# Optimization experiments

Hardware: AMD Instinct MI355X
Metric: run time of the kernel (lower is better)

## Reference

```python
import jax, jax.numpy as jnp
import numpy as np

N = 100000
NEG_SLOPE = 0.2
EPS = 1e-16


def _gat_layer(x, W, a_src, a_dst, b, src, dst, heads, dim, concat):
    # Linear projection -> [N, H, D]
    h = (x @ W).reshape(x.shape[0], heads, dim)
    # Per-node attention logits [N, H]
    al_src = jnp.sum(h * a_src[None], axis=-1)
    al_dst = jnp.sum(h * a_dst[None], axis=-1)
    # Per-edge logits, leaky relu (negative_slope=0.2)
    e = al_src[src] + al_dst[dst]                      # [E, H]
    e = jnp.where(e >= 0, e, NEG_SLOPE * e)
    # Scatter softmax over destination neighborhoods
    emax = jax.ops.segment_max(e, dst, num_segments=N)  # [N, H]
    ee = jnp.exp(e - emax[dst])
    denom = jax.ops.segment_sum(ee, dst, num_segments=N)
    alpha = ee / (denom[dst] + EPS)                    # [E, H]
    # Weighted scatter-add aggregation
    msg = h[src] * alpha[:, :, None]                   # [E, H, D]
    out = jax.ops.segment_sum(msg, dst, num_segments=N)  # [N, H, D]
    if concat:
        out = out.reshape(N, heads * dim)
    else:
        out = out.mean(axis=1)
    return out + b


def setup_inputs() -> dict:
    key = jax.random.key(0)
    ks = jax.random.split(key, 10)
    F_in, hid, H, C = 500, 8, 8, 3
    E = 3200000
    x = jax.random.normal(ks[0], (N, F_in), dtype=jnp.float32)
    edge_index = jax.random.randint(ks[1], (2, E), 0, N, dtype=jnp.int64)
    s1 = (1.0 / np.sqrt(F_in)).astype(np.float32)
    s2 = (1.0 / np.sqrt(hid * H)).astype(np.float32)
    return {
        "x": x,
        "edge_index": edge_index,
        "W1": jax.random.normal(ks[2], (F_in, H * hid), dtype=jnp.float32) * s1,
        "att_src1": jax.random.normal(ks[3], (H, hid), dtype=jnp.float32),
        "att_dst1": jax.random.normal(ks[4], (H, hid), dtype=jnp.float32),
        "b1": jnp.zeros((H * hid,), dtype=jnp.float32),
        "W2": jax.random.normal(ks[5], (H * hid, C), dtype=jnp.float32) * s2,
        "att_src2": jax.random.normal(ks[6], (1, C), dtype=jnp.float32),
        "att_dst2": jax.random.normal(ks[7], (1, C), dtype=jnp.float32),
        "b2": jnp.zeros((C,), dtype=jnp.float32),
    }


def reference(x, edge_index, W1, att_src1, att_dst1, b1, W2, att_src2, att_dst2, b2):
    # Add self-loops (PyG GATConv default)
    loop = jnp.arange(N, dtype=edge_index.dtype)
    src = jnp.concatenate([edge_index[0], loop])
    dst = jnp.concatenate([edge_index[1], loop])
    # Layer 1: 8 heads, concat -> [N, 64], ELU
    h = _gat_layer(x, W1, att_src1, att_dst1, b1, src, dst, heads=8, dim=8, concat=True)
    h = jax.nn.elu(h)
    # Layer 2: 1 head, no concat -> [N, 3]
    out = _gat_layer(h, W2, att_src2, att_dst2, b2, src, dst, heads=1, dim=3, concat=False)
    return out, jax.nn.log_softmax(out, axis=1)
```

## Files before the change

kernel.cpp:

```cpp
#include <hip/hip_runtime.h>
#include <hip/hip_bf16.h>


#define F_IN 500
#define HEADS 8
#define HID 8
#define HD 64
#define CLS 3
#define NEG 0.2f
#define EPSV 1e-16f
#define LOG2E 1.44269504088896340736f

#define NBLK_H 256
#define NBKT_MAX 3136

typedef __attribute__((ext_vector_type(8))) short short8v;
typedef __attribute__((ext_vector_type(4))) float f32x4;

__device__ inline short bfs(float v) {
    __hip_bfloat16 b = __float2bfloat16(v);
    return *(short*)&b;
}

__device__ inline int ld_edge(const void* ei, long idx, int is64) {
    return is64 ? (int)((const long long*)ei)[idx] : ((const int*)ei)[idx];
}

__global__ void k_prepW(const float* __restrict__ W1, ushort* __restrict__ W1b2,
                        const int* __restrict__ ei, int* __restrict__ flag) {
    if (blockIdx.x == 0 && threadIdx.x == 0) {
        int z = 0;
        for (int i = 1; i < 16; i += 2) z += (ei[i] == 0) ? 1 : 0;
        *flag = (z == 8) ? 1 : 0;
    }
    int i = blockIdx.x * 256 + threadIdx.x;
    if (i >= 16 * 64 * 32) return;
    int ks = i >> 11;
    int c = (i >> 5) & 63;
    int st = i & 31;
    int q = (st >> 3) ^ ((c >> 1) & 3);
    int k = ks * 32 + q * 8 + (st & 7);
    float v = (k < F_IN) ? W1[k * HD + c] : 0.f;
    __hip_bfloat16 b = __float2bfloat16(v);
    W1b2[i] = *(ushort*)&b;
}

__device__ __forceinline__ void g1_stage(const float* __restrict__ x,
        const ushort* __restrict__ W1b2, char* smem, int buf, int ks,
        int rowb, int N, int lane, int w) {
    const int k0 = ks * 32;
    {
        const ushort* srcB = W1b2 + ks * 2048 + (w * 64 + lane) * 8;
        char* dstB = smem + 16384 + buf * 4096 + w * 1024;
        __builtin_amdgcn_global_load_lds(
            (const __attribute__((address_space(1))) void*)srcB,
            (__attribute__((address_space(3))) void*)dstB, 16, 0, 0);
    }
#pragma unroll
    for (int i = 0; i < 2; ++i) {
        int vt = i * 256 + w * 64 + lane;
        int row = vt >> 3;
        int c = (vt & 7) ^ (row & 7);
        int ke = k0 + c * 4; if (ke > 496) ke = 496;
        int rowg = rowb + row; if (rowg >= N) rowg = N - 1;
        const float* srcA = x + (long)rowg * F_IN + ke;
        char* dstA = smem + buf * 8192 + i * 4096 + w * 1024;
        __builtin_amdgcn_global_load_lds(
            (const __attribute__((address_space(1))) void*)srcA,
            (__attribute__((address_space(3))) void*)dstA, 16, 0, 0);
    }
}

__global__ __launch_bounds__(256) void k_fatA(const float* __restrict__ x,
        const ushort* __restrict__ W1b2,
        const float* __restrict__ asrc, const float* __restrict__ adst,
        float* __restrict__ als, float* __restrict__ ald,
        ushort* __restrict__ h1b, int N,
        const void* ei, int E, int nbkt, int* __restrict__ ghist,
        const int* __restrict__ flag) {
    __shared__ char smem[24576];
    int gB = (N + 63) >> 6;
    int t = threadIdx.x;

    if ((int)blockIdx.x >= gB) {
        int hb = blockIdx.x - gB;
        int* h = (int*)smem;
        int tot = E + N;
        int epb = (tot + NBLK_H - 1) / NBLK_H;
        int e0 = hb * epb, e1 = min(tot, e0 + epb);
        for (int i = t; i < nbkt; i += 256) h[i] = 0;
        __syncthreads();
        int is64 = *flag;
        for (int e = e0 + t; e < e1; e += 256) {
            int dst = (e < E) ? ld_edge(ei, (long)E + e, is64) : (e - E);
            atomicAdd(&h[dst >> 5], 1);
        }
        __syncthreads();
        for (int i = t; i < nbkt; i += 256)
            ghist[hb * nbkt + i] = h[i];
        return;
    }

    int lane = t & 63;
    int w = t >> 6;
    int l16 = lane & 15, oct = lane >> 4;
    int rowb = blockIdx.x * 64;

    f32x4 acc0 = {0.f, 0.f, 0.f, 0.f};
    f32x4 acc1 = {0.f, 0.f, 0.f, 0.f};
    f32x4 acc2 = {0.f, 0.f, 0.f, 0.f};
    f32x4 acc3 = {0.f, 0.f, 0.f, 0.f};

    g1_stage(x, W1b2, smem, 0, 0, rowb, N, lane, w);
    __syncthreads();

    int rl = w * 16 + l16;
    int asw = l16 & 7;
    int bsw = (l16 >> 1) & 3;

    for (int ks = 0; ks < 16; ++ks) {
        int cur = ks & 1;
        if (ks < 15)
            g1_stage(x, W1b2, smem, cur ^ 1, ks + 1, rowb, N, lane, w);
        const char* Ab = smem + cur * 8192;
        const char* Bb = smem + 16384 + cur * 4096;
        float4 x0 = *reinterpret_cast<const float4*>(
            Ab + rl * 128 + ((2 * oct + 0) ^ asw) * 16);
        float4 x1 = *reinterpret_cast<const float4*>(
            Ab + rl * 128 + ((2 * oct + 1) ^ asw) * 16);
        short8v a;
        a[0] = bfs(x0.x); a[1] = bfs(x0.y); a[2] = bfs(x0.z); a[3] = bfs(x0.w);
        a[4] = bfs(x1.x); a[5] = bfs(x1.y); a[6] = bfs(x1.z); a[7] = bfs(x1.w);
        short8v b0 = *reinterpret_cast<const short8v*>(
            Bb + (0 * 16 + l16) * 64 + (oct ^ bsw) * 16);
        short8v b1 = *reinterpret_cast<const short8v*>(
            Bb + (1 * 16 + l16) * 64 + (oct ^ bsw) * 16);
        short8v b2 = *reinterpret_cast<const short8v*>(
            Bb + (2 * 16 + l16) * 64 + (oct ^ bsw) * 16);
        short8v b3 = *reinterpret_cast<const short8v*>(
            Bb + (3 * 16 + l16) * 64 + (oct ^ bsw) * 16);
        acc0 = __builtin_amdgcn_mfma_f32_16x16x32_bf16(a, b0, acc0, 0, 0, 0);
        acc1 = __builtin_amdgcn_mfma_f32_16x16x32_bf16(a, b1, acc1, 0, 0, 0);
        acc2 = __builtin_amdgcn_mfma_f32_16x16x32_bf16(a, b2, acc2, 0, 0, 0);
        acc3 = __builtin_amdgcn_mfma_f32_16x16x32_bf16(a, b3, acc3, 0, 0, 0);
        __syncthreads();
    }

    float* fs = (float*)smem;
#pragma unroll
    for (int r = 0; r < 4; ++r) {
        int rl_ = w * 16 + oct * 4 + r;
        fs[rl_ * 64 + l16 +  0] = acc0[r];
        fs[rl_ * 64 + l16 + 16] = acc1[r];
        fs[rl_ * 64 + l16 + 32] = acc2[r];
        fs[rl_ * 64 + l16 + 48] = acc3[r];
    }
    __syncthreads();
#pragma unroll
    for (int j = t; j < 512; j += 256) {
        int row = j >> 3, h = j & 7;
        int gn = rowb + row;
        if (gn < N) {
            const float* hp = fs + row * 64 + h * 8;
            float4 v0 = *reinterpret_cast<const float4*>(hp);
            float4 v1 = *reinterpret_cast<const float4*>(hp + 4);
            const float* s = asrc + h * 8;
            const float* d = adst + h * 8;
            float s1 = v0.x * s[0] + v0.y * s[1] + v0.z * s[2] + v0.w * s[3]
                     + v1.x * s[4] + v1.y * s[5] + v1.z * s[6] + v1.w * s[7];
            float s2 = v0.x * d[0] + v0.y * d[1] + v0.z * d[2] + v0.w * d[3]
                     + v1.x * d[4] + v1.y * d[5] + v1.z * d[6] + v1.w * d[7];
            als[gn * 8 + h] = s1 * LOG2E;
            ald[gn * 8 + h] = s2 * LOG2E;
            ushort hb[8];
            hb[0] = (ushort)bfs(v0.x); hb[1] = (ushort)bfs(v0.y);
            hb[2] = (ushort)bfs(v0.z); hb[3] = (ushort)bfs(v0.w);
            hb[4] = (ushort)bfs(v1.x); hb[5] = (ushort)bfs(v1.y);
            hb[6] = (ushort)bfs(v1.z); hb[7] = (ushort)bfs(v1.w);
            *reinterpret_cast<uint4*>(h1b + (long)gn * HD + h * 8) =
                *reinterpret_cast<const uint4*>(hb);
        }
    }
}


__global__ void k_bsum(const int* __restrict__ ghist, int* __restrict__ colsum, int nbkt) {
    int b = blockIdx.x * 256 + threadIdx.x;
    if (b >= nbkt) return;
    int s = 0;
    for (int i = 0; i < NBLK_H; i++) s += ghist[i * nbkt + b];
    colsum[b] = s;
}

__global__ __launch_bounds__(256) void k_bscan2(const int* __restrict__ colsum,
        int* __restrict__ boff, int nbkt) {
    __shared__ int part[256];
    int per = (nbkt + 255) / 256;
    int t = threadIdx.x;
    int lo = t * per, hi = min(nbkt, lo + per);
    int s = 0;
    for (int i = lo; i < hi; i++) s += colsum[i];
    part[t] = s;
    __syncthreads();
    for (int off = 1; off < 256; off <<= 1) {
        int v = (t >= off) ? part[t - off] : 0;
        __syncthreads();
        part[t] += v;
        __syncthreads();
    }
    int run = (t > 0) ? part[t - 1] : 0;
    for (int i = lo; i < hi; i++) { boff[i] = run; run += colsum[i]; }
    if (t == 255) boff[nbkt] = part[255];
}

__global__ void k_bapply(int* __restrict__ ghist, const int* __restrict__ boff, int nbkt) {
    int b = blockIdx.x * 256 + threadIdx.x;
    if (b >= nbkt) return;
    int run = boff[b];
    for (int i = 0; i < NBLK_H; i++) {
        int v = ghist[i * nbkt + b];
        ghist[i * nbkt + b] = run;
        run += v;
    }
}

__global__ __launch_bounds__(256) void k_scatter(const void* ei, int E, int N, int nbkt,
        const int* __restrict__ ghist, uint* __restrict__ pairs, const int* flag) {
    __shared__ int cur[NBKT_MAX];
    int tot = E + N;
    int epb = (tot + NBLK_H - 1) / NBLK_H;
    int e0 = blockIdx.x * epb, e1 = min(tot, e0 + epb);
    for (int i = threadIdx.x; i < nbkt; i += 256) cur[i] = ghist[blockIdx.x * nbkt + i];
    __syncthreads();
    int is64 = *flag;
    for (int e = e0 + threadIdx.x; e < e1; e += 256) {
        int src, dst;
        if (e < E) { src = ld_edge(ei, e, is64); dst = ld_edge(ei, (long)E + e, is64); }
        else { src = dst = e - E; }
        int pos = atomicAdd(&cur[dst >> 5], 1);
        pairs[pos] = ((uint)src << 5) | (uint)(dst & 31);
    }
}

__global__ __launch_bounds__(256) void k_fill3(const uint* __restrict__ pairs,
        const int* __restrict__ boff, int* __restrict__ rowptr,
        int* __restrict__ csr, int N, int nbkt) {
    __shared__ int cnt[32];
    __shared__ int base[32];
    __shared__ int cur[32];
    int b = blockIdx.x;
    int t = threadIdx.x;
    if (t < 32) { cnt[t] = 0; cur[t] = 0; }
    __syncthreads();
    int p0 = boff[b], p1 = boff[b + 1];
    for (int p = p0 + t; p < p1; p += 256)
        atomicAdd(&cnt[pairs[p] & 31], 1);
    __syncthreads();
    if (t < 32) {
        int pre = 0;
#pragma unroll
        for (int i = 0; i < 32; i++) pre += (i < t) ? cnt[i] : 0;
        base[t] = p0 + pre;
        int n = b * 32 + t;
        if (n < N) rowptr[n] = base[t];
    }
    if (b == 0 && t == 0) rowptr[N] = boff[nbkt];
    __syncthreads();
    for (int p = p0 + t; p < p1; p += 256) {
        uint v = pairs[p];
        int lo = v & 31;
        int pos = base[lo] + atomicAdd(&cur[lo], 1);
        csr[pos] = (int)(v >> 5);
    }
}

__global__ __launch_bounds__(256) void k_agg1(const int* __restrict__ rowptr,
        const int* __restrict__ csr, const ushort* __restrict__ h1b,
        const float* __restrict__ als, const float* __restrict__ ald,
        const float* __restrict__ b1, const float* __restrict__ W2,
        const float* __restrict__ as2, const float* __restrict__ ad2,
        float* __restrict__ h2p, float* __restrict__ als2,
        float* __restrict__ ald2, int N) {
    int n = blockIdx.x * 4 + (threadIdx.x >> 6);
    if (n >= N) return;
    int lane = threadIdx.x & 63;
    int es = lane >> 3;
    int h = lane & 7;
    float aldh = ald[n * HEADS + h];
    int rs = rowptr[n], re = rowptr[n + 1];

    float acc[4][8];
    float den[4] = {0.f, 0.f, 0.f, 0.f};
#pragma unroll
    for (int q = 0; q < 4; ++q)
#pragma unroll
        for (int j = 0; j < 8; ++j) acc[q][j] = 0.f;

    int jb = rs;
    for (; jb + 32 <= re; jb += 32) {
        int s[4]; float e[4]; float p[4]; uint4 u[4];
#pragma unroll
        for (int q = 0; q < 4; ++q) s[q] = csr[jb + q * 8 + es];
#pragma unroll
        for (int q = 0; q < 4; ++q) {
            e[q] = als[s[q] * HEADS + h] + aldh;
            u[q] = *reinterpret_cast<const uint4*>(h1b + (long)s[q] * HD + h * 8);
        }
#pragma unroll
        for (int q = 0; q < 4; ++q) {
            e[q] = fmaxf(e[q], NEG * e[q]);
            p[q] = exp2f(e[q]);
        }
#pragma unroll
        for (int q = 0; q < 4; ++q) {
            acc[q][0] += p[q] * __uint_as_float(u[q].x << 16);
            acc[q][1] += p[q] * __uint_as_float(u[q].x & 0xffff0000u);
            acc[q][2] += p[q] * __uint_as_float(u[q].y << 16);
            acc[q][3] += p[q] * __uint_as_float(u[q].y & 0xffff0000u);
            acc[q][4] += p[q] * __uint_as_float(u[q].z << 16);
            acc[q][5] += p[q] * __uint_as_float(u[q].z & 0xffff0000u);
            acc[q][6] += p[q] * __uint_as_float(u[q].w << 16);
            acc[q][7] += p[q] * __uint_as_float(u[q].w & 0xffff0000u);
            den[q] += p[q];
        }
    }
    for (; jb + 16 <= re; jb += 16) {
        int s[2]; float e[2]; float p[2]; uint4 u[2];
#pragma unroll
        for (int q = 0; q < 2; ++q) s[q] = csr[jb + q * 8 + es];
#pragma unroll
        for (int q = 0; q < 2; ++q) {
            e[q] = als[s[q] * HEADS + h] + aldh;
            u[q] = *reinterpret_cast<const uint4*>(h1b + (long)s[q] * HD + h * 8);
        }
#pragma unroll
        for (int q = 0; q < 2; ++q) {
            e[q] = fmaxf(e[q], NEG * e[q]);
            p[q] = exp2f(e[q]);
        }
#pragma unroll
        for (int q = 0; q < 2; ++q) {
            acc[q][0] += p[q] * __uint_as_float(u[q].x << 16);
            acc[q][1] += p[q] * __uint_as_float(u[q].x & 0xffff0000u);
            acc[q][2] += p[q] * __uint_as_float(u[q].y << 16);
            acc[q][3] += p[q] * __uint_as_float(u[q].y & 0xffff0000u);
            acc[q][4] += p[q] * __uint_as_float(u[q].z << 16);
            acc[q][5] += p[q] * __uint_as_float(u[q].z & 0xffff0000u);
            acc[q][6] += p[q] * __uint_as_float(u[q].w << 16);
            acc[q][7] += p[q] * __uint_as_float(u[q].w & 0xffff0000u);
            den[q] += p[q];
        }
    }
    for (; jb < re; jb += 8) {
        int eidx = jb + es;
        bool valid = (eidx < re);
        int s = csr[valid ? eidx : rs];
        float e = als[s * HEADS + h] + aldh;
        e = fmaxf(e, NEG * e);
        float p = valid ? exp2f(e) : 0.f;
        uint4 u = *reinterpret_cast<const uint4*>(h1b + (long)s * HD + h * 8);
        acc[0][0] += p * __uint_as_float(u.x << 16);
        acc[0][1] += p * __uint_as_float(u.x & 0xffff0000u);
        acc[0][2] += p * __uint_as_float(u.y << 16);
        acc[0][3] += p * __uint_as_float(u.y & 0xffff0000u);
        acc[0][4] += p * __uint_as_float(u.z << 16);
        acc[0][5] += p * __uint_as_float(u.z & 0xffff0000u);
        acc[0][6] += p * __uint_as_float(u.w << 16);
        acc[0][7] += p * __uint_as_float(u.w & 0xffff0000u);
        den[0] += p;
    }
    float a0 = (acc[0][0] + acc[1][0]) + (acc[2][0] + acc[3][0]);
    float a1 = (acc[0][1] + acc[1][1]) + (acc[2][1] + acc[3][1]);
    float a2 = (acc[0][2] + acc[1][2]) + (acc[2][2] + acc[3][2]);
    float a3 = (acc[0][3] + acc[1][3]) + (acc[2][3] + acc[3][3]);
    float a4 = (acc[0][4] + acc[1][4]) + (acc[2][4] + acc[3][4]);
    float a5 = (acc[0][5] + acc[1][5]) + (acc[2][5] + acc[3][5]);
    float a6 = (acc[0][6] + acc[1][6]) + (acc[2][6] + acc[3][6]);
    float a7 = (acc[0][7] + acc[1][7]) + (acc[2][7] + acc[3][7]);
    float dn = (den[0] + den[1]) + (den[2] + den[3]);
#pragma unroll
    for (int off = 8; off < 64; off <<= 1) {
        dn += __shfl_xor(dn, off);
        a0 += __shfl_xor(a0, off); a1 += __shfl_xor(a1, off);
        a2 += __shfl_xor(a2, off); a3 += __shfl_xor(a3, off);
        a4 += __shfl_xor(a4, off); a5 += __shfl_xor(a5, off);
        a6 += __shfl_xor(a6, off); a7 += __shfl_xor(a7, off);
    }
    float sel = (es < 4)
        ? ((es < 2) ? ((es == 0) ? a0 : a1) : ((es == 2) ? a2 : a3))
        : ((es < 6) ? ((es == 4) ? a4 : a5) : ((es == 6) ? a6 : a7));
    int d = h * 8 + es;
    float o = sel / (dn + EPSV) + b1[d];
    o = (o > 0.f) ? o : __expf(o) - 1.f;
    float p0 = o * W2[d * CLS + 0];
    float p1 = o * W2[d * CLS + 1];
    float p2 = o * W2[d * CLS + 2];
#pragma unroll
    for (int off = 1; off < 64; off <<= 1) {
        p0 += __shfl_xor(p0, off);
        p1 += __shfl_xor(p1, off);
        p2 += __shfl_xor(p2, off);
    }
    if (lane == 0) {
        *reinterpret_cast<float4*>(h2p + (long)n * 4) = make_float4(p0, p1, p2, 0.f);
        als2[n] = (p0 * as2[0] + p1 * as2[1] + p2 * as2[2]) * LOG2E;
        ald2[n] = (p0 * ad2[0] + p1 * ad2[1] + p2 * ad2[2]) * LOG2E;
    }
}

__global__ __launch_bounds__(256) void k_agg2(const int* __restrict__ rowptr,
        const int* __restrict__ csr, const float* __restrict__ h2p,
        const float* __restrict__ als2v, const float* __restrict__ ald2v,
        const float* __restrict__ b2, float* __restrict__ out, int N) {
    int n = blockIdx.x * 8 + (threadIdx.x >> 5);
    if (n >= N) return;
    int lane = threadIdx.x & 31;
    float aldv = ald2v[n];
    int rs = rowptr[n], re = rowptr[n + 1];
    float sum = 0.f, a0 = 0.f, a1 = 0.f, a2 = 0.f;
    for (int j = rs + lane; j < re; j += 32) {
        int s = csr[j];
        float e = als2v[s] + aldv;
        e = fmaxf(e, NEG * e);
        float p = exp2f(e);
        float4 hv = *reinterpret_cast<const float4*>(h2p + (long)s * 4);
        sum += p;
        a0 += p * hv.x;
        a1 += p * hv.y;
        a2 += p * hv.z;
    }
#pragma unroll
    for (int off = 1; off < 32; off <<= 1) {
        sum += __shfl_xor(sum, off);
        a0 += __shfl_xor(a0, off);
        a1 += __shfl_xor(a1, off);
        a2 += __shfl_xor(a2, off);
    }
    if (lane == 0) {
        float d = sum + EPSV;
        float v0 = a0 / d + b2[0], v1 = a1 / d + b2[1], v2 = a2 / d + b2[2];
        float mx = fmaxf(v0, fmaxf(v1, v2));
        float se = __expf(v0 - mx) + __expf(v1 - mx) + __expf(v2 - mx);
        float ls = mx + __logf(se);
        out[n * CLS + 0] = v0; out[n * CLS + 1] = v1; out[n * CLS + 2] = v2;
        long o2 = (long)N * CLS;
        out[o2 + n * CLS + 0] = v0 - ls;
        out[o2 + n * CLS + 1] = v1 - ls;
        out[o2 + n * CLS + 2] = v2 - ls;
    }
}

extern "C" void kernel_launch(void* const* d_in, const int* in_sizes, int n_in,
                              void* d_out, int out_size, void* d_ws, size_t ws_size,
                              hipStream_t stream) {
    const float* x   = (const float*)d_in[0];
    const void*  ei  = d_in[1];
    const float* W1  = (const float*)d_in[2];
    const float* as1 = (const float*)d_in[3];
    const float* ad1 = (const float*)d_in[4];
    const float* b1  = (const float*)d_in[5];
    const float* W2  = (const float*)d_in[6];
    const float* as2 = (const float*)d_in[7];
    const float* ad2 = (const float*)d_in[8];
    const float* b2  = (const float*)d_in[9];
    int N = in_sizes[0] / F_IN;
    int E = in_sizes[1] / 2;
    int tot = E + N;
    int nbkt = (N + 31) >> 5;

    char* w = (char*)d_ws;
    auto alloc = [&](size_t bytes) -> char* {
        char* p = w; w += (bytes + 255) & ~size_t(255); return p;
    };
    ushort* h1b    = (ushort*)alloc((size_t)N * HD * 2);
    float*  als1   = (float*)alloc((size_t)N * HEADS * 4);
    float*  ald1   = (float*)alloc((size_t)N * HEADS * 4);
    int*    rowptr = (int*)alloc((size_t)(N + 1) * 4);
    int*    csr    = (int*)alloc((size_t)tot * 4);
    float*  h2p    = (float*)alloc((size_t)N * 4 * 4);
    float*  als2   = (float*)alloc((size_t)N * 4);
    float*  ald2   = (float*)alloc((size_t)N * 4);
    ushort* W1b2   = (ushort*)alloc((size_t)16 * 64 * 32 * 2);
    int*    flag   = (int*)alloc(256);
    uint*   pairs  = (uint*)alloc((size_t)tot * 4);
    int*    ghist  = (int*)alloc((size_t)NBLK_H * nbkt * 4);
    int*    colsum = (int*)alloc((size_t)nbkt * 4);
    int*    boff   = (int*)alloc((size_t)(nbkt + 1) * 4);

    int gB = (N + 63) / 64;
    k_prepW<<<(16 * 64 * 32 + 255) / 256, 256, 0, stream>>>(W1, W1b2, (const int*)ei, flag);
    k_fatA<<<gB + NBLK_H, 256, 0, stream>>>(x, W1b2, as1, ad1, als1, ald1, h1b, N,
                                            ei, E, nbkt, ghist, flag);
    k_bsum<<<(nbkt + 255) / 256, 256, 0, stream>>>(ghist, colsum, nbkt);
    k_bscan2<<<1, 256, 0, stream>>>(colsum, boff, nbkt);
    k_bapply<<<(nbkt + 255) / 256, 256, 0, stream>>>(ghist, boff, nbkt);
    k_scatter<<<NBLK_H, 256, 0, stream>>>(ei, E, N, nbkt, ghist, pairs, flag);
    k_fill3<<<nbkt, 256, 0, stream>>>(pairs, boff, rowptr, csr, N, nbkt);
    k_agg1<<<(N + 3) / 4, 256, 0, stream>>>(rowptr, csr, h1b, als1, ald1, b1,
                                            W2, as2, ad2, h2p, als2, ald2, N);
    k_agg2<<<(N + 7) / 8, 256, 0, stream>>>(rowptr, csr, h2p, als2, ald2, b2,
                                            (float*)d_out, N);
}
```

Before: 306.7 us.

## Recompute source attention logits from gathered bf16 features instead of gathering als

Layer 1 no longer precomputes and stores per-node source logits. The aggregation kernel instead recomputes them from the bf16 h1 vector it already gathers, as an 8-wide dot product with att_src. This removes one dependent random gather per edge and the als write/read traffic, at the cost of extra FMAs and slightly different numerics, since bf16 features now feed the logits. Layer 2 packs its source logit into the unused fourth slot of h2p, so one float4 gather serves both values. The 16-edge remainder loop is also dropped, so leftover edges now go through the 8-wide tail loop.

```diff
diff --git a/kernel.cpp b/kernel.cpp
--- a/kernel.cpp
+++ b/kernel.cpp
@@ -73,8 +73,8 @@
 
 __global__ __launch_bounds__(256) void k_fatA(const float* __restrict__ x,
         const ushort* __restrict__ W1b2,
-        const float* __restrict__ asrc, const float* __restrict__ adst,
-        float* __restrict__ als, float* __restrict__ ald,
+        const float* __restrict__ adst,
+        float* __restrict__ ald,
         ushort* __restrict__ h1b, int N,
         const void* ei, int E, int nbkt, int* __restrict__ ghist,
         const int* __restrict__ flag) {
@@ -164,13 +164,9 @@
             const float* hp = fs + row * 64 + h * 8;
             float4 v0 = *reinterpret_cast<const float4*>(hp);
             float4 v1 = *reinterpret_cast<const float4*>(hp + 4);
-            const float* s = asrc + h * 8;
             const float* d = adst + h * 8;
-            float s1 = v0.x * s[0] + v0.y * s[1] + v0.z * s[2] + v0.w * s[3]
-                     + v1.x * s[4] + v1.y * s[5] + v1.z * s[6] + v1.w * s[7];
             float s2 = v0.x * d[0] + v0.y * d[1] + v0.z * d[2] + v0.w * d[3]
                      + v1.x * d[4] + v1.y * d[5] + v1.z * d[6] + v1.w * d[7];
-            als[gn * 8 + h] = s1 * LOG2E;
             ald[gn * 8 + h] = s2 * LOG2E;
             ushort hb[8];
             hb[0] = (ushort)bfs(v0.x); hb[1] = (ushort)bfs(v0.y);
@@ -276,17 +272,19 @@
 
 __global__ __launch_bounds__(256) void k_agg1(const int* __restrict__ rowptr,
         const int* __restrict__ csr, const ushort* __restrict__ h1b,
-        const float* __restrict__ als, const float* __restrict__ ald,
+        const float* __restrict__ asrc, const float* __restrict__ ald,
         const float* __restrict__ b1, const float* __restrict__ W2,
         const float* __restrict__ as2, const float* __restrict__ ad2,
-        float* __restrict__ h2p, float* __restrict__ als2,
-        float* __restrict__ ald2, int N) {
+        float* __restrict__ h2p, float* __restrict__ ald2, int N) {
     int n = blockIdx.x * 4 + (threadIdx.x >> 6);
     if (n >= N) return;
     int lane = threadIdx.x & 63;
     int es = lane >> 3;
     int h = lane & 7;
     float aldh = ald[n * HEADS + h];
+    float asc[8];
+#pragma unroll
+    for (int j = 0; j < 8; ++j) asc[j] = asrc[h * 8 + j] * LOG2E;
     int rs = rowptr[n], re = rowptr[n + 1];
 
     float acc[4][8];
@@ -298,75 +296,56 @@
 
     int jb = rs;
     for (; jb + 32 <= re; jb += 32) {
-        int s[4]; float e[4]; float p[4]; uint4 u[4];
+        int s[4]; uint4 u[4];
 #pragma unroll
         for (int q = 0; q < 4; ++q) s[q] = csr[jb + q * 8 + es];
 #pragma unroll
+        for (int q = 0; q < 4; ++q)
+            u[q] = *reinterpret_cast<const uint4*>(h1b + (long)s[q] * HD + h * 8);
+#pragma unroll
         for (int q = 0; q < 4; ++q) {
-            e[q] = als[s[q] * HEADS + h] + aldh;
-            u[q] = *reinterpret_cast<const uint4*>(h1b + (long)s[q] * HD + h * 8);
-        }
-#pragma unroll
-        for (int q = 0; q < 4; ++q) {
-            e[q] = fmaxf(e[q], NEG * e[q]);
-            p[q] = exp2f(e[q]);
-        }
-#pragma unroll
-        for (int q = 0; q < 4; ++q) {
-            acc[q][0] += p[q] * __uint_as_float(u[q].x << 16);
-            acc[q][1] += p[q] * __uint_as_float(u[q].x & 0xffff0000u);
-            acc[q][2] += p[q] * __uint_as_float(u[q].y << 16);
-            acc[q][3] += p[q] * __uint_as_float(u[q].y & 0xffff0000u);
-            acc[q][4] += p[q] * __uint_as_float(u[q].z << 16);
-            acc[q][5] += p[q] * __uint_as_float(u[q].z & 0xffff0000u);
-            acc[q][6] += p[q] * __uint_as_float(u[q].w << 16);
-            acc[q][7] += p[q] * __uint_as_float(u[q].w & 0xffff0000u);
-            den[q] += p[q];
-        }
-    }
-    for (; jb + 16 <= re; jb += 16) {
-        int s[2]; float e[2]; float p[2]; uint4 u[2];
-#pragma unroll
-        for (int q = 0; q < 2; ++q) s[q] = csr[jb + q * 8 + es];
-#pragma unroll
-        for (int q = 0; q < 2; ++q) {
-            e[q] = als[s[q] * HEADS + h] + aldh;
-            u[q] = *reinterpret_cast<const uint4*>(h1b + (long)s[q] * HD + h * 8);
-        }
-#pragma unroll
-        for (int q = 0; q < 2; ++q) {
-            e[q] = fmaxf(e[q], NEG * e[q]);
-            p[q] = exp2f(e[q]);
-        }
-#pragma unroll
-        for (int q = 0; q < 2; ++q) {
-            acc[q][0] += p[q] * __uint_as_float(u[q].x << 16);
-            acc[q][1] += p[q] * __uint_as_float(u[q].x & 0xffff0000u);
-            acc[q][2] += p[q] * __uint_as_float(u[q].y << 16);
-            acc[q][3] += p[q] * __uint_as_float(u[q].y & 0xffff0000u);
-            acc[q][4] += p[q] * __uint_as_float(u[q].z << 16);
-            acc[q][5] += p[q] * __uint_as_float(u[q].z & 0xffff0000u);
-            acc[q][6] += p[q] * __uint_as_float(u[q].w << 16);
-            acc[q][7] += p[q] * __uint_as_float(u[q].w & 0xffff0000u);
-            den[q] += p[q];
+            float f0 = __uint_as_float(u[q].x << 16);
+            float f1 = __uint_as_float(u[q].x & 0xffff0000u);
+            float f2 = __uint_as_float(u[q].y << 16);
+            float f3 = __uint_as_float(u[q].y & 0xffff0000u);
+            float f4 = __uint_as_float(u[q].z << 16);
+            float f5 = __uint_as_float(u[q].z & 0xffff0000u);
+            float f6 = __uint_as_float(u[q].w << 16);
+            float f7 = __uint_as_float(u[q].w & 0xffff0000u);
+            float e = ((f0 * asc[0] + f1 * asc[1]) + (f2 * asc[2] + f3 * asc[3]))
+                    + ((f4 * asc[4] + f5 * asc[5]) + (f6 * asc[6] + f7 * asc[7]))
+                    + aldh;
+            e = fmaxf(e, NEG * e);
+            float p = exp2f(e);
+            acc[q][0] += p * f0; acc[q][1] += p * f1;
+            acc[q][2] += p * f2; acc[q][3] += p * f3;
+            acc[q][4] += p * f4; acc[q][5] += p * f5;
+            acc[q][6] += p * f6; acc[q][7] += p * f7;
+            den[q] += p;
         }
     }
     for (; jb < re; jb += 8) {
         int eidx = jb + es;
         bool valid = (eidx < re);
         int s = csr[valid ? eidx : rs];
-        float e = als[s * HEADS + h] + aldh;
+        uint4 u = *reinterpret_cast<const uint4*>(h1b + (long)s * HD + h * 8);
+        float f0 = __uint_as_float(u.x << 16);
+        float f1 = __uint_as_float(u.x & 0xffff0000u);
+        float f2 = __uint_as_float(u.y << 16);
+        float f3 = __uint_as_float(u.y & 0xffff0000u);
+        float f4 = __uint_as_float(u.z << 16);
+        float f5 = __uint_as_float(u.z & 0xffff0000u);
+        float f6 = __uint_as_float(u.w << 16);
+        float f7 = __uint_as_float(u.w & 0xffff0000u);
+        float e = ((f0 * asc[0] + f1 * asc[1]) + (f2 * asc[2] + f3 * asc[3]))
+                + ((f4 * asc[4] + f5 * asc[5]) + (f6 * asc[6] + f7 * asc[7]))
+                + aldh;
         e = fmaxf(e, NEG * e);
         float p = valid ? exp2f(e) : 0.f;
-        uint4 u = *reinterpret_cast<const uint4*>(h1b + (long)s * HD + h * 8);
-        acc[0][0] += p * __uint_as_float(u.x << 16);
-        acc[0][1] += p * __uint_as_float(u.x & 0xffff0000u);
-        acc[0][2] += p * __uint_as_float(u.y << 16);
-        acc[0][3] += p * __uint_as_float(u.y & 0xffff0000u);
-        acc[0][4] += p * __uint_as_float(u.z << 16);
-        acc[0][5] += p * __uint_as_float(u.z & 0xffff0000u);
-        acc[0][6] += p * __uint_as_float(u.w << 16);
-        acc[0][7] += p * __uint_as_float(u.w & 0xffff0000u);
+        acc[0][0] += p * f0; acc[0][1] += p * f1;
+        acc[0][2] += p * f2; acc[0][3] += p * f3;
+        acc[0][4] += p * f4; acc[0][5] += p * f5;
+        acc[0][6] += p * f6; acc[0][7] += p * f7;
         den[0] += p;
     }
     float a0 = (acc[0][0] + acc[1][0]) + (acc[2][0] + acc[3][0]);
@@ -402,15 +381,16 @@
         p2 += __shfl_xor(p2, off);
     }
     if (lane == 0) {
-        *reinterpret_cast<float4*>(h2p + (long)n * 4) = make_float4(p0, p1, p2, 0.f);
-        als2[n] = (p0 * as2[0] + p1 * as2[1] + p2 * as2[2]) * LOG2E;
+        float als2v = (p0 * as2[0] + p1 * as2[1] + p2 * as2[2]) * LOG2E;
+        *reinterpret_cast<float4*>(h2p + (long)n * 4) =
+            make_float4(p0, p1, p2, als2v);
         ald2[n] = (p0 * ad2[0] + p1 * ad2[1] + p2 * ad2[2]) * LOG2E;
     }
 }
 
 __global__ __launch_bounds__(256) void k_agg2(const int* __restrict__ rowptr,
         const int* __restrict__ csr, const float* __restrict__ h2p,
-        const float* __restrict__ als2v, const float* __restrict__ ald2v,
+        const float* __restrict__ ald2v,
         const float* __restrict__ b2, float* __restrict__ out, int N) {
     int n = blockIdx.x * 8 + (threadIdx.x >> 5);
     if (n >= N) return;
@@ -420,10 +400,10 @@
     float sum = 0.f, a0 = 0.f, a1 = 0.f, a2 = 0.f;
     for (int j = rs + lane; j < re; j += 32) {
         int s = csr[j];
-        float e = als2v[s] + aldv;
+        float4 hv = *reinterpret_cast<const float4*>(h2p + (long)s * 4);
+        float e = hv.w + aldv;
         e = fmaxf(e, NEG * e);
         float p = exp2f(e);
-        float4 hv = *reinterpret_cast<const float4*>(h2p + (long)s * 4);
         sum += p;
         a0 += p * hv.x;
         a1 += p * hv.y;
@@ -473,12 +453,10 @@
         char* p = w; w += (bytes + 255) & ~size_t(255); return p;
     };
     ushort* h1b    = (ushort*)alloc((size_t)N * HD * 2);
-    float*  als1   = (float*)alloc((size_t)N * HEADS * 4);
     float*  ald1   = (float*)alloc((size_t)N * HEADS * 4);
     int*    rowptr = (int*)alloc((size_t)(N + 1) * 4);
     int*    csr    = (int*)alloc((size_t)tot * 4);
     float*  h2p    = (float*)alloc((size_t)N * 4 * 4);
-    float*  als2   = (float*)alloc((size_t)N * 4);
     float*  ald2   = (float*)alloc((size_t)N * 4);
     ushort* W1b2   = (ushort*)alloc((size_t)16 * 64 * 32 * 2);
     int*    flag   = (int*)alloc(256);
@@ -489,15 +467,15 @@
 
     int gB = (N + 63) / 64;
     k_prepW<<<(16 * 64 * 32 + 255) / 256, 256, 0, stream>>>(W1, W1b2, (const int*)ei, flag);
-    k_fatA<<<gB + NBLK_H, 256, 0, stream>>>(x, W1b2, as1, ad1, als1, ald1, h1b, N,
+    k_fatA<<<gB + NBLK_H, 256, 0, stream>>>(x, W1b2, ad1, ald1, h1b, N,
                                             ei, E, nbkt, ghist, flag);
     k_bsum<<<(nbkt + 255) / 256, 256, 0, stream>>>(ghist, colsum, nbkt);
     k_bscan2<<<1, 256, 0, stream>>>(colsum, boff, nbkt);
     k_bapply<<<(nbkt + 255) / 256, 256, 0, stream>>>(ghist, boff, nbkt);
     k_scatter<<<NBLK_H, 256, 0, stream>>>(ei, E, N, nbkt, ghist, pairs, flag);
     k_fill3<<<nbkt, 256, 0, stream>>>(pairs, boff, rowptr, csr, N, nbkt);
-    k_agg1<<<(N + 3) / 4, 256, 0, stream>>>(rowptr, csr, h1b, als1, ald1, b1,
-                                            W2, as2, ad2, h2p, als2, ald2, N);
-    k_agg2<<<(N + 7) / 8, 256, 0, stream>>>(rowptr, csr, h2p, als2, ald2, b2,
+    k_agg1<<<(N + 3) / 4, 256, 0, stream>>>(rowptr, csr, h1b, as1, ald1, b1,
+                                            W2, as2, ad2, h2p, ald2, N);
+    k_agg2<<<(N + 7) / 8, 256, 0, stream>>>(rowptr, csr, h2p, ald2, b2,
                                             (float*)d_out, N);
 }
```

After: 314.5 us. 1.03x slower.

## Use half-wavefront per node in agg1 and pack als2 into h2p padding

Applied to the files above, without the earlier changes.

The layer-1 aggregation now assigns 32 lanes per destination node instead of 64, processing two nodes per wavefront with 4 edge slots per head. Average degree is about 32, so the old full-wave path mostly hit the remainder loops. The change also drops a shuffle stage and splits the final reduction across two feature columns per lane. The layer-2 source logit is stored in the unused fourth float of h2p, so agg2 gets it from the same float4 gather and one separate array and its random loads go away.

```diff
diff --git a/kernel.cpp b/kernel.cpp
--- a/kernel.cpp
+++ b/kernel.cpp
@@ -279,15 +279,17 @@
         const float* __restrict__ als, const float* __restrict__ ald,
         const float* __restrict__ b1, const float* __restrict__ W2,
         const float* __restrict__ as2, const float* __restrict__ ad2,
-        float* __restrict__ h2p, float* __restrict__ als2,
-        float* __restrict__ ald2, int N) {
-    int n = blockIdx.x * 4 + (threadIdx.x >> 6);
-    if (n >= N) return;
+        float* __restrict__ h2p, float* __restrict__ ald2, int N) {
     int lane = threadIdx.x & 63;
-    int es = lane >> 3;
+    int wid = threadIdx.x >> 6;
+    int half = lane >> 5;
+    int n = blockIdx.x * 8 + wid * 2 + half;
+    bool act = (n < N);
+    int nc = act ? n : (N - 1);
+    int es = (lane >> 3) & 3;
     int h = lane & 7;
-    float aldh = ald[n * HEADS + h];
-    int rs = rowptr[n], re = rowptr[n + 1];
+    float aldh = ald[nc * HEADS + h];
+    int rs = rowptr[nc], re = rowptr[nc + 1];
 
     float acc[4][8];
     float den[4] = {0.f, 0.f, 0.f, 0.f};
@@ -297,10 +299,10 @@
         for (int j = 0; j < 8; ++j) acc[q][j] = 0.f;
 
     int jb = rs;
-    for (; jb + 32 <= re; jb += 32) {
+    for (; jb + 16 <= re; jb += 16) {
         int s[4]; float e[4]; float p[4]; uint4 u[4];
 #pragma unroll
-        for (int q = 0; q < 4; ++q) s[q] = csr[jb + q * 8 + es];
+        for (int q = 0; q < 4; ++q) s[q] = csr[jb + q * 4 + es];
 #pragma unroll
         for (int q = 0; q < 4; ++q) {
             e[q] = als[s[q] * HEADS + h] + aldh;
@@ -324,34 +326,7 @@
             den[q] += p[q];
         }
     }
-    for (; jb + 16 <= re; jb += 16) {
-        int s[2]; float e[2]; float p[2]; uint4 u[2];
-#pragma unroll
-        for (int q = 0; q < 2; ++q) s[q] = csr[jb + q * 8 + es];
-#pragma unroll
-        for (int q = 0; q < 2; ++q) {
-            e[q] = als[s[q] * HEADS + h] + aldh;
-            u[q] = *reinterpret_cast<const uint4*>(h1b + (long)s[q] * HD + h * 8);
-        }
-#pragma unroll
-        for (int q = 0; q < 2; ++q) {
-            e[q] = fmaxf(e[q], NEG * e[q]);
-            p[q] = exp2f(e[q]);
-        }
-#pragma unroll
-        for (int q = 0; q < 2; ++q) {
-            acc[q][0] += p[q] * __uint_as_float(u[q].x << 16);
-            acc[q][1] += p[q] * __uint_as_float(u[q].x & 0xffff0000u);
-            acc[q][2] += p[q] * __uint_as_float(u[q].y << 16);
-            acc[q][3] += p[q] * __uint_as_float(u[q].y & 0xffff0000u);
-            acc[q][4] += p[q] * __uint_as_float(u[q].z << 16);
-            acc[q][5] += p[q] * __uint_as_float(u[q].z & 0xffff0000u);
-            acc[q][6] += p[q] * __uint_as_float(u[q].w << 16);
-            acc[q][7] += p[q] * __uint_as_float(u[q].w & 0xffff0000u);
-            den[q] += p[q];
-        }
-    }
-    for (; jb < re; jb += 8) {
+    for (; jb < re; jb += 4) {
         int eidx = jb + es;
         bool valid = (eidx < re);
         int s = csr[valid ? eidx : rs];
@@ -379,38 +354,41 @@
     float a7 = (acc[0][7] + acc[1][7]) + (acc[2][7] + acc[3][7]);
     float dn = (den[0] + den[1]) + (den[2] + den[3]);
 #pragma unroll
-    for (int off = 8; off < 64; off <<= 1) {
+    for (int off = 8; off <= 16; off <<= 1) {
         dn += __shfl_xor(dn, off);
         a0 += __shfl_xor(a0, off); a1 += __shfl_xor(a1, off);
         a2 += __shfl_xor(a2, off); a3 += __shfl_xor(a3, off);
         a4 += __shfl_xor(a4, off); a5 += __shfl_xor(a5, off);
         a6 += __shfl_xor(a6, off); a7 += __shfl_xor(a7, off);
     }
-    float sel = (es < 4)
-        ? ((es < 2) ? ((es == 0) ? a0 : a1) : ((es == 2) ? a2 : a3))
-        : ((es < 6) ? ((es == 4) ? a4 : a5) : ((es == 6) ? a6 : a7));
-    int d = h * 8 + es;
-    float o = sel / (dn + EPSV) + b1[d];
-    o = (o > 0.f) ? o : __expf(o) - 1.f;
-    float p0 = o * W2[d * CLS + 0];
-    float p1 = o * W2[d * CLS + 1];
-    float p2 = o * W2[d * CLS + 2];
-#pragma unroll
-    for (int off = 1; off < 64; off <<= 1) {
+    float sel_a = (es < 2) ? ((es == 0) ? a0 : a1) : ((es == 2) ? a2 : a3);
+    float sel_b = (es < 2) ? ((es == 0) ? a4 : a5) : ((es == 2) ? a6 : a7);
+    int da = h * 8 + es, db = da + 4;
+    float inv = 1.f / (dn + EPSV);
+    float oa = sel_a * inv + b1[da];
+    float ob = sel_b * inv + b1[db];
+    oa = (oa > 0.f) ? oa : __expf(oa) - 1.f;
+    ob = (ob > 0.f) ? ob : __expf(ob) - 1.f;
+    float p0 = oa * W2[da * CLS + 0] + ob * W2[db * CLS + 0];
+    float p1 = oa * W2[da * CLS + 1] + ob * W2[db * CLS + 1];
+    float p2 = oa * W2[da * CLS + 2] + ob * W2[db * CLS + 2];
+#pragma unroll
+    for (int off = 1; off <= 16; off <<= 1) {
         p0 += __shfl_xor(p0, off);
         p1 += __shfl_xor(p1, off);
         p2 += __shfl_xor(p2, off);
     }
-    if (lane == 0) {
-        *reinterpret_cast<float4*>(h2p + (long)n * 4) = make_float4(p0, p1, p2, 0.f);
-        als2[n] = (p0 * as2[0] + p1 * as2[1] + p2 * as2[2]) * LOG2E;
+    if ((lane & 31) == 0 && act) {
+        float als2v = (p0 * as2[0] + p1 * as2[1] + p2 * as2[2]) * LOG2E;
+        *reinterpret_cast<float4*>(h2p + (long)n * 4) =
+            make_float4(p0, p1, p2, als2v);
         ald2[n] = (p0 * ad2[0] + p1 * ad2[1] + p2 * ad2[2]) * LOG2E;
     }
 }
 
 __global__ __launch_bounds__(256) void k_agg2(const int* __restrict__ rowptr,
         const int* __restrict__ csr, const float* __restrict__ h2p,
-        const float* __restrict__ als2v, const float* __restrict__ ald2v,
+        const float* __restrict__ ald2v,
         const float* __restrict__ b2, float* __restrict__ out, int N) {
     int n = blockIdx.x * 8 + (threadIdx.x >> 5);
     if (n >= N) return;
@@ -420,10 +398,10 @@
     float sum = 0.f, a0 = 0.f, a1 = 0.f, a2 = 0.f;
     for (int j = rs + lane; j < re; j += 32) {
         int s = csr[j];
-        float e = als2v[s] + aldv;
+        float4 hv = *reinterpret_cast<const float4*>(h2p + (long)s * 4);
+        float e = hv.w + aldv;
         e = fmaxf(e, NEG * e);
         float p = exp2f(e);
-        float4 hv = *reinterpret_cast<const float4*>(h2p + (long)s * 4);
         sum += p;
         a0 += p * hv.x;
         a1 += p * hv.y;
@@ -478,7 +456,6 @@
     int*    rowptr = (int*)alloc((size_t)(N + 1) * 4);
     int*    csr    = (int*)alloc((size_t)tot * 4);
     float*  h2p    = (float*)alloc((size_t)N * 4 * 4);
-    float*  als2   = (float*)alloc((size_t)N * 4);
     float*  ald2   = (float*)alloc((size_t)N * 4);
     ushort* W1b2   = (ushort*)alloc((size_t)16 * 64 * 32 * 2);
     int*    flag   = (int*)alloc(256);
@@ -496,8 +473,8 @@
     k_bapply<<<(nbkt + 255) / 256, 256, 0, stream>>>(ghist, boff, nbkt);
     k_scatter<<<NBLK_H, 256, 0, stream>>>(ei, E, N, nbkt, ghist, pairs, flag);
     k_fill3<<<nbkt, 256, 0, stream>>>(pairs, boff, rowptr, csr, N, nbkt);
-    k_agg1<<<(N + 3) / 4, 256, 0, stream>>>(rowptr, csr, h1b, als1, ald1, b1,
-                                            W2, as2, ad2, h2p, als2, ald2, N);
-    k_agg2<<<(N + 7) / 8, 256, 0, stream>>>(rowptr, csr, h2p, als2, ald2, b2,
+    k_agg1<<<(N + 7) / 8, 256, 0, stream>>>(rowptr, csr, h1b, als1, ald1, b1,
+                                            W2, as2, ad2, h2p, ald2, N);
+    k_agg2<<<(N + 7) / 8, 256, 0, stream>>>(rowptr, csr, h2p, ald2, b2,
                                             (float*)d_out, N);
 }
```

Measured after the change: 285.1 us (median of 3 runs). -7.0%, faster.
